# Kernel tuning notes

Measured on AMD Instinct MI355X. Metric: run time of the kernel, lower is better.

Reference implementation:

```python
import jax, jax.numpy as jnp
import numpy as np

N, E, IN_DIM, H_DIM, T = 100000, 3200000, 128, 128, 5000


def gcn_conv(x, W, b, src, dst):
    """PyG GCNConv: symmetric norm with self-loops, linear transform, scatter-add."""
    n = x.shape[0]
    h = x @ W  # [N, h]
    # degree with self-loops (all edge weights = 1)
    deg = jax.ops.segment_sum(jnp.ones(src.shape[0], x.dtype), dst, num_segments=n) + 1.0
    dinv = jax.lax.rsqrt(deg)  # deg >= 1 due to self-loops
    norm = dinv[src] * dinv[dst]  # [E]
    out = jax.ops.segment_sum(h[src] * norm[:, None], dst, num_segments=n)
    out = out + h * (dinv * dinv)[:, None]  # self-loop contribution
    return out + b


def setup_inputs() -> dict:
    key = jax.random.key(0)
    ks = jax.random.split(key, 24)
    s_in = 1.0 / np.sqrt(IN_DIM)
    s_h = 1.0 / np.sqrt(H_DIM)
    return {
        "x": jax.random.normal(ks[0], (N, IN_DIM), jnp.float32),
        "edge_index": jax.random.randint(ks[1], (2, E), 0, N),
        "fake_x": jax.random.normal(ks[2], (N, IN_DIM), jnp.float32),
        "fake_edge_index": jax.random.randint(ks[3], (2, E), 0, N),
        "treat_idx": jax.random.randint(ks[4], (T,), 0, N),
        "control_idx": jax.random.randint(ks[5], (T,), 0, N),
        # GCN layer params
        "W1": jax.random.normal(ks[6], (IN_DIM, H_DIM), jnp.float32) * s_in,
        "b1": jnp.zeros((H_DIM,), jnp.float32),
        "W2": jax.random.normal(ks[7], (H_DIM, H_DIM), jnp.float32) * s_h,
        "b2": jnp.zeros((H_DIM,), jnp.float32),
        # heads
        "Wy1": jax.random.normal(ks[8], (H_DIM, 1), jnp.float32) * s_h,
        "by1": jnp.zeros((1,), jnp.float32),
        "Wy0": jax.random.normal(ks[9], (H_DIM, 1), jnp.float32) * s_h,
        "by0": jnp.zeros((1,), jnp.float32),
        "Wb": jax.random.normal(ks[10], (H_DIM, 2), jnp.float32) * s_h,
        "bb": jnp.zeros((2,), jnp.float32),
        "Wp1": jax.random.normal(ks[11], (H_DIM, H_DIM), jnp.float32) * s_h,
        "bp1": jnp.zeros((H_DIM,), jnp.float32),
        "Wp2": jax.random.normal(ks[12], (H_DIM, 2), jnp.float32) * s_h,
        "bp2": jnp.zeros((2,), jnp.float32),
    }


@jax.custom_vjp
def grl(x):
    return x

def _grl_fwd(x):
    return x, None

def _grl_bwd(_, g):
    return (-g,)

grl.defvjp(_grl_fwd, _grl_bwd)


def reference(x, edge_index, fake_x, fake_edge_index, treat_idx, control_idx,
              W1, b1, W2, b2, Wy1, by1, Wy0, by0, Wb, bb, Wp1, bp1, Wp2, bp2):
    lrelu = jax.nn.leaky_relu  # slope 0.01 matches torch default
    src, dst = edge_index[0], edge_index[1]
    fsrc, fdst = fake_edge_index[0], fake_edge_index[1]

    # layer 1 + relu (dropout is identity in eval mode)
    xZ1 = jax.nn.relu(gcn_conv(x, W1, b1, src, dst))
    xfZ1 = jax.nn.relu(gcn_conv(fake_x, W1, b1, fsrc, fdst))
    # layer 2
    xZ2 = gcn_conv(xZ1, W2, b2, src, dst)
    xfZ2 = gcn_conv(xfZ1, W2, b2, fsrc, fdst)

    y1 = lrelu(xZ2[treat_idx] @ Wy1 + by1).squeeze(-1)
    yc0 = lrelu(xfZ2[treat_idx] @ Wy0 + by0).squeeze(-1)
    y0 = lrelu(xZ2[control_idx] @ Wy0 + by0).squeeze(-1)
    yc1 = lrelu(xfZ2[control_idx] @ Wy1 + by1).squeeze(-1)

    fprob = grl(xZ2) @ Wb + bb
    fprob_f = grl(xfZ2) @ Wb + bb

    tprob = lrelu(lrelu(xZ2 @ Wp1 + bp1) @ Wp2 + bp2)
    tprob_f = lrelu(lrelu(xfZ2 @ Wp1 + bp1) @ Wp2 + bp2)

    return (y1, yc0, y0, yc1, fprob, fprob_f, tprob, tprob_f)
```

## Files before the change

kernel.cpp:

```cpp
#include <hip/hip_runtime.h>

#define DIM 128
#define EPB 8192
#define BINSH 8
#define BINN 256

typedef unsigned int uint32;
typedef __attribute__((ext_vector_type(8))) short short8;
typedef __attribute__((ext_vector_type(4))) float f32x4;

__device__ __forceinline__ uint32 bf16_rtne(float f) {
  uint32 u = __float_as_uint(f);
  return (u + 0x7FFFu + ((u >> 16) & 1u)) >> 16;
}
__device__ __forceinline__ float bf16_to_f(uint32 h) { return __uint_as_float(h << 16); }
__device__ __forceinline__ void unpack2(uint32 u, float& x, float& y) {
  x = __uint_as_float(u << 16);
  y = __uint_as_float(u & 0xFFFF0000u);
}


__launch_bounds__(256)
__global__ void csr_sort_kernel(const int* __restrict__ src, const int* __restrict__ dst,
                                int E, int nb1, uint32* __restrict__ tmp,
                                int* __restrict__ dir) {
  __shared__ uint32 sorted[EPB];
  __shared__ int lcnt[512];
  __shared__ int lbase[512];
  __shared__ int ps[256];
  int t = threadIdx.x;
  int base = blockIdx.x * EPB;

  lcnt[t] = 0;
  lcnt[t + 256] = 0;
  __syncthreads();

  uint32 val[32];
  uint32 br[32];
#pragma unroll
  for (int i = 0; i < 32; ++i) {
    int e = base + i * 256 + t;
    if (e < E) {
      int d = __builtin_nontemporal_load(dst + e);
      int s = __builtin_nontemporal_load(src + e);
      int bin = d >> BINSH;
      val[i] = ((uint32)s << BINSH) | (uint32)(d & (BINN - 1));
      int rank = atomicAdd(&lcnt[bin], 1);
      br[i] = ((uint32)bin << 13) | (uint32)rank;
    } else {
      br[i] = 0xFFFFFFFFu;
    }
  }
  __syncthreads();

  {
    int a0 = lcnt[2 * t], a1 = lcnt[2 * t + 1];
    int psum = a0 + a1;
    ps[t] = psum;
    __syncthreads();
    for (int off = 1; off < 256; off <<= 1) {
      int x = (t >= off) ? ps[t - off] : 0;
      __syncthreads();
      ps[t] += x;
      __syncthreads();
    }
    int ebase = ps[t] - psum;
    lbase[2 * t] = ebase;
    lbase[2 * t + 1] = ebase + a0;
  }
  __syncthreads();

#pragma unroll
  for (int i = 0; i < 32; ++i) {
    if (br[i] != 0xFFFFFFFFu) {
      int bin = br[i] >> 13;
      int rank = br[i] & 0x1FFF;
      sorted[lbase[bin] + rank] = val[i];
    }
  }
  __syncthreads();

  int cnt = min(EPB, E - base);
#pragma unroll
  for (int i = 0; i < 32; ++i) {
    int idx = i * 256 + t;
    if (idx < cnt) tmp[base + idx] = sorted[idx];
  }
  for (int b = t; b <= nb1; b += 256) {
    dir[blockIdx.x * (nb1 + 1) + b] = lbase[b];
  }
}


__launch_bounds__(256)
__global__ void csr_build_kernel(const uint32* __restrict__ tmp, const int* __restrict__ dir,
                                 int nA, int nb1, int N, int binCap,
                                 int* __restrict__ row_beg, int* __restrict__ row_end,
                                 int* __restrict__ cols, float* __restrict__ dinv) {
  __shared__ int rbeg[512];
  __shared__ int rend[512];
  __shared__ int deg[BINN];
  __shared__ int cur[BINN];
  __shared__ int ps[256];
  int j = blockIdx.x;
  int t = threadIdx.x;
  int node0 = j << BINSH;
  int colsBase = j * binCap;

  if (t < BINN) deg[t] = 0;
  for (int i = t; i < nA; i += 256) {
    rbeg[i] = dir[i * (nb1 + 1) + j];
    rend[i] = dir[i * (nb1 + 1) + j + 1];
  }
  __syncthreads();

  for (int i = t; i < nA; i += 256) {
    int b = rbeg[i], en = rend[i];
    for (int q = b; q < en; ++q) {
      atomicAdd(&deg[tmp[(size_t)i * EPB + q] & (BINN - 1)], 1);
    }
  }
  __syncthreads();

  int dv = deg[t];
  ps[t] = dv;
  __syncthreads();
  for (int off = 1; off < 256; off <<= 1) {
    int x = (t >= off) ? ps[t - off] : 0;
    __syncthreads();
    ps[t] += x;
    __syncthreads();
  }
  int ebase = ps[t] - dv;
  cur[t] = ebase;
  int node = node0 + t;
  if (node < N) {
    row_beg[node] = colsBase + ebase;
    row_end[node] = colsBase + ebase + dv;
    dinv[node] = rsqrtf((float)dv + 1.0f);
  }
  __syncthreads();

  for (int i = t; i < nA; i += 256) {
    int b = rbeg[i], en = rend[i];
    for (int q = b; q < en; ++q) {
      uint32 v = tmp[(size_t)i * EPB + q];
      int p = atomicAdd(&cur[v & (BINN - 1)], 1);
      cols[colsBase + p] = (int)(v >> BINSH);
    }
  }
}


__global__ void wsplit_kernel(const float* __restrict__ W, uint4* __restrict__ hi4,
                              uint4* __restrict__ lo4) {
  int tid = blockIdx.x * blockDim.x + threadIdx.x;
  int lane = tid & 63;
  int ks = (tid >> 6) & 3;
  int ct = tid >> 8;
  int col = ct * 16 + (lane & 15);
  int k0 = ks * 32 + ((lane >> 4) << 3);
  uint32 h[8], l[8];
#pragma unroll
  for (int j = 0; j < 8; ++j) {
    float w = W[(size_t)(k0 + j) * DIM + col];
    uint32 hh = bf16_rtne(w);
    float rem = w - bf16_to_f(hh);
    l[j] = bf16_rtne(rem);
    h[j] = hh;
  }
  uint4 H, L;
  H.x = h[0] | (h[1] << 16); H.y = h[2] | (h[3] << 16);
  H.z = h[4] | (h[5] << 16); H.w = h[6] | (h[7] << 16);
  L.x = l[0] | (l[1] << 16); L.y = l[2] | (l[3] << 16);
  L.z = l[4] | (l[5] << 16); L.w = l[6] | (l[7] << 16);
  hi4[tid] = H;
  lo4[tid] = L;
}


__launch_bounds__(256, 3)
__global__ void gemm_mfma_kernel(const float* __restrict__ in, const uint4* __restrict__ wHi,
                                 const uint4* __restrict__ wLo, uint32* __restrict__ outb,
                                 int n, const float* __restrict__ rowscale,
                                 const float* __restrict__ bias, float slope,
                                 const float* __restrict__ headW,
                                 const float* __restrict__ headB,
                                 float* __restrict__ headOut) {
  __shared__ unsigned short sA[2 * 64 * 128];
  __shared__ unsigned short sO[64 * 128];
  int t = threadIdx.x;
  int row0 = blockIdx.x * 64;

  {
    int quad = t & 31;
    int r = t >> 5;
#pragma unroll
    for (int i = 0; i < 8; ++i) {
      int row = r + i * 8;
      int grow = row0 + row;
      f32x4 v = (f32x4){0.f, 0.f, 0.f, 0.f};
      if (grow < n) v = *(const f32x4*)(in + (size_t)grow * DIM + quad * 4);
      uint32 h0 = bf16_rtne(v.x), h1 = bf16_rtne(v.y), h2 = bf16_rtne(v.z), h3 = bf16_rtne(v.w);
      uint32 l0 = bf16_rtne(v.x - bf16_to_f(h0));
      uint32 l1 = bf16_rtne(v.y - bf16_to_f(h1));
      uint32 l2 = bf16_rtne(v.z - bf16_to_f(h2));
      uint32 l3 = bf16_rtne(v.w - bf16_to_f(h3));
      int sidx = (row * 128 + quad * 4) ^ ((row & 7) << 3);
      *(uint2*)&sA[sidx] = make_uint2(h0 | (h1 << 16), h2 | (h3 << 16));
      *(uint2*)&sA[64 * 128 + sidx] = make_uint2(l0 | (l1 << 16), l2 | (l3 << 16));
    }
  }
  __syncthreads();

  int lane = t & 63;
  int w = t >> 6;
  int rbase = w * 16;
  f32x4 acc[8];
#pragma unroll
  for (int ct = 0; ct < 8; ++ct) acc[ct] = (f32x4){0.f, 0.f, 0.f, 0.f};

  int fragRow = rbase + (lane & 15);
  int fragSwz = (fragRow & 7) << 3;
#pragma unroll
  for (int ks = 0; ks < 4; ++ks) {
    int cidx = ks * 32 + ((lane >> 4) << 3);
    int sidx = (fragRow * 128 + cidx) ^ fragSwz;
    uint4 au = *(uint4*)&sA[sidx];
    uint4 alu = *(uint4*)&sA[64 * 128 + sidx];
    short8 ah = __builtin_bit_cast(short8, au);
    short8 al = __builtin_bit_cast(short8, alu);
#pragma unroll
    for (int ct = 0; ct < 8; ++ct) {
      int widx = (ct * 4 + ks) * 64 + lane;
      short8 bh = __builtin_bit_cast(short8, wHi[widx]);
      short8 bl = __builtin_bit_cast(short8, wLo[widx]);
      acc[ct] = __builtin_amdgcn_mfma_f32_16x16x32_bf16(al, bh, acc[ct], 0, 0, 0);
      acc[ct] = __builtin_amdgcn_mfma_f32_16x16x32_bf16(ah, bl, acc[ct], 0, 0, 0);
      acc[ct] = __builtin_amdgcn_mfma_f32_16x16x32_bf16(ah, bh, acc[ct], 0, 0, 0);
    }
  }

  float rs[4];
#pragma unroll
  for (int r = 0; r < 4; ++r) {
    int grow = row0 + rbase + ((lane >> 4) << 2) + r;
    rs[r] = rowscale ? ((grow < n) ? rowscale[grow] : 0.f) : 1.0f;
  }

  float hp0[4] = {0.f, 0.f, 0.f, 0.f};
  float hp1[4] = {0.f, 0.f, 0.f, 0.f};

#pragma unroll
  for (int ct = 0; ct < 8; ++ct) {
    int col = ct * 16 + (lane & 15);
    float bv = bias ? bias[col] : 0.f;
    float hw0 = 0.f, hw1 = 0.f;
    if (headOut) {
      hw0 = headW[col * 2 + 0];
      hw1 = headW[col * 2 + 1];
    }
#pragma unroll
    for (int r = 0; r < 4; ++r) {
      int rowL = rbase + ((lane >> 4) << 2) + r;
      float v = acc[ct][r] * rs[r] + bv;
      v = (v > 0.f) ? v : v * slope;
      if (outb) {
        int sidx = (rowL * 128 + col) ^ ((rowL & 7) << 3);
        sO[sidx] = (unsigned short)bf16_rtne(v);
      }
      if (headOut) {
        hp0[r] = fmaf(v, hw0, hp0[r]);
        hp1[r] = fmaf(v, hw1, hp1[r]);
      }
    }
  }

  if (headOut) {
    float hb0 = headB[0], hb1 = headB[1];
#pragma unroll
    for (int r = 0; r < 4; ++r) {
      float a = hp0[r], b = hp1[r];
#pragma unroll
      for (int off = 8; off; off >>= 1) {
        a += __shfl_xor(a, off);
        b += __shfl_xor(b, off);
      }
      if ((lane & 15) == 0) {
        int grow = row0 + rbase + ((lane >> 4) << 2) + r;
        if (grow < n) {
          float o0 = a + hb0, o1 = b + hb1;
          headOut[2 * (size_t)grow + 0] = (o0 > 0.f) ? o0 : 0.01f * o0;
          headOut[2 * (size_t)grow + 1] = (o1 > 0.f) ? o1 : 0.01f * o1;
        }
      }
    }
  }

  if (outb) {
    __syncthreads();
#pragma unroll
    for (int it = 0; it < 4; ++it) {
      int s = it * 64 + lane;
      int row = rbase + (s >> 4);
      int sin = s & 15;
      int sidx = row * 128 + ((sin * 8) ^ ((row & 7) << 3));
      uint4 v = *(uint4*)&sO[sidx];
      int grow = row0 + row;
      if (grow < n) *(uint4*)(outb + (size_t)grow * 64 + sin * 4) = v;
    }
  }
}


__launch_bounds__(256)
__global__ void agg_kernel(const uint32* __restrict__ g, const int* __restrict__ row_beg,
                           const int* __restrict__ row_end, const int* __restrict__ cols,
                           const float* __restrict__ dinv, const float* __restrict__ bias,
                           float* __restrict__ out, int n, int relu,
                           const float* __restrict__ fpW, const float* __restrict__ fpB,
                           float* __restrict__ fpOut) {
  int lane = threadIdx.x & 63;
  int node = (blockIdx.x * blockDim.x + threadIdx.x) >> 6;
  if (node >= n) return;
  int beg = row_beg[node];
  int end = row_end[node];
  float ax, ay;
  unpack2(g[(size_t)node * 64 + lane], ax, ay);
  float bx = 0.f, by = 0.f;
  int e = beg;
  for (; e + 8 <= end; e += 8) {
    int s0 = cols[e + 0], s1 = cols[e + 1], s2 = cols[e + 2], s3 = cols[e + 3];
    int s4 = cols[e + 4], s5 = cols[e + 5], s6 = cols[e + 6], s7 = cols[e + 7];
    uint32 u0 = g[(size_t)s0 * 64 + lane];
    uint32 u1 = g[(size_t)s1 * 64 + lane];
    uint32 u2 = g[(size_t)s2 * 64 + lane];
    uint32 u3 = g[(size_t)s3 * 64 + lane];
    uint32 u4 = g[(size_t)s4 * 64 + lane];
    uint32 u5 = g[(size_t)s5 * 64 + lane];
    uint32 u6 = g[(size_t)s6 * 64 + lane];
    uint32 u7 = g[(size_t)s7 * 64 + lane];
    float x0, y0, x1, y1, x2, y2, x3, y3, x4, y4, x5, y5, x6, y6, x7, y7;
    unpack2(u0, x0, y0); unpack2(u1, x1, y1);
    unpack2(u2, x2, y2); unpack2(u3, x3, y3);
    unpack2(u4, x4, y4); unpack2(u5, x5, y5);
    unpack2(u6, x6, y6); unpack2(u7, x7, y7);
    ax += (x0 + x1) + (x2 + x3);
    ay += (y0 + y1) + (y2 + y3);
    bx += (x4 + x5) + (x6 + x7);
    by += (y4 + y5) + (y6 + y7);
  }
  for (; e < end; ++e) {
    uint32 u0 = g[(size_t)cols[e] * 64 + lane];
    float x0, y0;
    unpack2(u0, x0, y0);
    ax += x0;
    ay += y0;
  }
  ax += bx;
  ay += by;
  float di = dinv[node];
  float2 bv = ((const float2*)bias)[lane];
  float ox = fmaf(di, ax, bv.x);
  float oy = fmaf(di, ay, bv.y);
  if (relu) {
    ox = fmaxf(ox, 0.f);
    oy = fmaxf(oy, 0.f);
  }
  ((float2*)out)[(size_t)node * 64 + lane] = make_float2(ox, oy);

  if (fpOut) {
    float w00 = fpW[(2 * lane) * 2 + 0];
    float w01 = fpW[(2 * lane) * 2 + 1];
    float w10 = fpW[(2 * lane + 1) * 2 + 0];
    float w11 = fpW[(2 * lane + 1) * 2 + 1];
    float p0 = ox * w00 + oy * w10;
    float p1 = ox * w01 + oy * w11;
#pragma unroll
    for (int off = 32; off; off >>= 1) {
      p0 += __shfl_xor(p0, off);
      p1 += __shfl_xor(p1, off);
    }
    if (lane == 0) {
      fpOut[2 * (size_t)node + 0] = p0 + fpB[0];
      fpOut[2 * (size_t)node + 1] = p1 + fpB[1];
    }
  }
}


__global__ void ydot_kernel(const float* __restrict__ Z, const int* __restrict__ idx,
                            const float* __restrict__ w, const float* __restrict__ b,
                            float* __restrict__ out, int T) {
  int lane = threadIdx.x & 63;
  int t = (blockIdx.x * blockDim.x + threadIdx.x) >> 6;
  if (t >= T) return;
  float2 wv = ((const float2*)w)[lane];
  int node = idx[t];
  float2 z = ((const float2*)Z)[(size_t)node * 64 + lane];
  float pp = z.x * wv.x + z.y * wv.y;
#pragma unroll
  for (int off = 32; off; off >>= 1) pp += __shfl_xor(pp, off);
  if (lane == 0) {
    float o = pp + b[0];
    out[t] = (o > 0.f) ? o : 0.01f * o;
  }
}


extern "C" void kernel_launch(void* const* d_in, const int* in_sizes, int n_in,
                              void* d_out, int out_size, void* d_ws, size_t ws_size,
                              hipStream_t stream) {
  const int N = in_sizes[0] / DIM;
  const int E = in_sizes[1] / 2;
  const int T = in_sizes[4];
  const int nb1 = (N + BINN - 1) >> BINSH;
  const int nA = (E + EPB - 1) / EPB;
  const int binCap = ((E / nb1 + 1024 + 15) / 16) * 16;

  const float* x = (const float*)d_in[0];
  const int* ei = (const int*)d_in[1];
  const float* fx = (const float*)d_in[2];
  const int* fei = (const int*)d_in[3];
  const int* treat = (const int*)d_in[4];
  const int* control = (const int*)d_in[5];
  const float* W1 = (const float*)d_in[6];
  const float* b1 = (const float*)d_in[7];
  const float* W2 = (const float*)d_in[8];
  const float* b2 = (const float*)d_in[9];
  const float* Wy1 = (const float*)d_in[10];
  const float* by1 = (const float*)d_in[11];
  const float* Wy0 = (const float*)d_in[12];
  const float* by0 = (const float*)d_in[13];
  const float* Wb = (const float*)d_in[14];
  const float* bb = (const float*)d_in[15];
  const float* Wp1 = (const float*)d_in[16];
  const float* bp1 = (const float*)d_in[17];
  const float* Wp2 = (const float*)d_in[18];
  const float* bp2 = (const float*)d_in[19];

  float* out = (float*)d_out;

  char* p = (char*)d_ws;
  float* bufZ = (float*)p;   p += (size_t)N * DIM * sizeof(float);
  uint32* bufG = (uint32*)p; p += (size_t)N * (DIM / 2) * sizeof(uint32);
  int* cols = (int*)p;       p += (size_t)nb1 * binCap * sizeof(int);
  int* dir = (int*)p;        p += (size_t)nA * (nb1 + 1) * sizeof(int);
  int* row_beg = (int*)p;    p += (size_t)(N + 16) * sizeof(int);
  int* row_end = (int*)p;    p += (size_t)(N + 16) * sizeof(int);
  float* dinv = (float*)p;   p += (size_t)(N + 16) * sizeof(float);
  uint4* w1Hi = (uint4*)p;   p += 2048 * sizeof(uint4);
  uint4* w1Lo = (uint4*)p;   p += 2048 * sizeof(uint4);
  uint4* w2Hi = (uint4*)p;   p += 2048 * sizeof(uint4);
  uint4* w2Lo = (uint4*)p;   p += 2048 * sizeof(uint4);
  uint4* wp1Hi = (uint4*)p;  p += 2048 * sizeof(uint4);
  uint4* wp1Lo = (uint4*)p;  p += 2048 * sizeof(uint4);
  uint32* tmp = (uint32*)bufZ;

  float* oy1 = out;
  float* oyc0 = out + T;
  float* oy0 = out + 2 * T;
  float* oyc1 = out + 3 * T;
  float* ofp = out + 4 * T;
  float* ofpf = out + 4 * T + 2 * N;
  float* otp = out + 4 * T + 4 * N;
  float* otpf = out + 4 * T + 6 * N;

  wsplit_kernel<<<8, 256, 0, stream>>>(W1, w1Hi, w1Lo);
  wsplit_kernel<<<8, 256, 0, stream>>>(W2, w2Hi, w2Lo);
  wsplit_kernel<<<8, 256, 0, stream>>>(Wp1, wp1Hi, wp1Lo);

  auto run = [&](const float* X, const int* EI,
                 float* y_t, const float* Wt, const float* bt,
                 float* y_c, const float* Wc, const float* bc,
                 float* fp, float* tp) {
    const int* srcp = EI;
    const int* dstp = EI + E;
    csr_sort_kernel<<<nA, 256, 0, stream>>>(srcp, dstp, E, nb1, tmp, dir);
    csr_build_kernel<<<nb1, 256, 0, stream>>>(tmp, dir, nA, nb1, N, binCap,
                                              row_beg, row_end, cols, dinv);
    gemm_mfma_kernel<<<(N + 63) / 64, 256, 0, stream>>>(X, w1Hi, w1Lo, bufG, N, dinv,
                                                        nullptr, 1.0f, nullptr, nullptr, nullptr);
    agg_kernel<<<(N + 3) / 4, 256, 0, stream>>>(bufG, row_beg, row_end, cols, dinv, b1,
                                                bufZ, N, 1, nullptr, nullptr, nullptr);
    gemm_mfma_kernel<<<(N + 63) / 64, 256, 0, stream>>>(bufZ, w2Hi, w2Lo, bufG, N, dinv,
                                                        nullptr, 1.0f, nullptr, nullptr, nullptr);
    agg_kernel<<<(N + 3) / 4, 256, 0, stream>>>(bufG, row_beg, row_end, cols, dinv, b2,
                                                bufZ, N, 0, Wb, bb, fp);
    gemm_mfma_kernel<<<(N + 63) / 64, 256, 0, stream>>>(bufZ, wp1Hi, wp1Lo, nullptr, N, nullptr,
                                                        bp1, 0.01f, Wp2, bp2, tp);
    ydot_kernel<<<(T + 3) / 4, 256, 0, stream>>>(bufZ, treat, Wt, bt, y_t, T);
    ydot_kernel<<<(T + 3) / 4, 256, 0, stream>>>(bufZ, control, Wc, bc, y_c, T);
  };

  run(x, ei, oy1, Wy1, by1, oy0, Wy0, by0, ofp, otp);
  run(fx, fei, oyc0, Wy0, by0, oyc1, Wy1, by1, ofpf, otpf);
}
```

Before: 888.5 us.

## Store layer-1 activations as bf16 and skip lo-split MFMA in layer-2 GEMM

```diff
diff --git a/kernel.cpp b/kernel.cpp
--- a/kernel.cpp
+++ b/kernel.cpp
@@ -183,7 +183,7 @@
 __global__ void gemm_mfma_kernel(const float* __restrict__ in, const uint4* __restrict__ wHi,
                                  const uint4* __restrict__ wLo, uint32* __restrict__ outb,
                                  int n, const float* __restrict__ rowscale,
-                                 const float* __restrict__ bias, float slope,
+                                 const float* __restrict__ bias, float slope, int in_bf16,
                                  const float* __restrict__ headW,
                                  const float* __restrict__ headB,
                                  float* __restrict__ headOut) {
@@ -192,7 +192,20 @@
   int t = threadIdx.x;
   int row0 = blockIdx.x * 64;
 
-  {
+  if (in_bf16) {
+    const uint4* in4 = (const uint4*)in;
+    int q = t & 15;
+    int rl = t >> 4;
+#pragma unroll
+    for (int i = 0; i < 4; ++i) {
+      int row = rl + i * 16;
+      int grow = row0 + row;
+      uint4 v = make_uint4(0, 0, 0, 0);
+      if (grow < n) v = in4[(size_t)grow * 16 + q];
+      int sidx = (row * 128 + q * 8) ^ ((row & 7) << 3);
+      *(uint4*)&sA[sidx] = v;
+    }
+  } else {
     int quad = t & 31;
     int r = t >> 5;
 #pragma unroll
@@ -227,15 +240,15 @@
     int cidx = ks * 32 + ((lane >> 4) << 3);
     int sidx = (fragRow * 128 + cidx) ^ fragSwz;
     uint4 au = *(uint4*)&sA[sidx];
-    uint4 alu = *(uint4*)&sA[64 * 128 + sidx];
     short8 ah = __builtin_bit_cast(short8, au);
-    short8 al = __builtin_bit_cast(short8, alu);
+    short8 al;
+    if (!in_bf16) al = __builtin_bit_cast(short8, *(uint4*)&sA[64 * 128 + sidx]);
 #pragma unroll
     for (int ct = 0; ct < 8; ++ct) {
       int widx = (ct * 4 + ks) * 64 + lane;
       short8 bh = __builtin_bit_cast(short8, wHi[widx]);
       short8 bl = __builtin_bit_cast(short8, wLo[widx]);
-      acc[ct] = __builtin_amdgcn_mfma_f32_16x16x32_bf16(al, bh, acc[ct], 0, 0, 0);
+      if (!in_bf16) acc[ct] = __builtin_amdgcn_mfma_f32_16x16x32_bf16(al, bh, acc[ct], 0, 0, 0);
       acc[ct] = __builtin_amdgcn_mfma_f32_16x16x32_bf16(ah, bl, acc[ct], 0, 0, 0);
       acc[ct] = __builtin_amdgcn_mfma_f32_16x16x32_bf16(ah, bh, acc[ct], 0, 0, 0);
     }
@@ -317,7 +330,7 @@
 __global__ void agg_kernel(const uint32* __restrict__ g, const int* __restrict__ row_beg,
                            const int* __restrict__ row_end, const int* __restrict__ cols,
                            const float* __restrict__ dinv, const float* __restrict__ bias,
-                           float* __restrict__ out, int n, int relu,
+                           void* __restrict__ out, int n, int relu, int out_bf16,
                            const float* __restrict__ fpW, const float* __restrict__ fpB,
                            float* __restrict__ fpOut) {
   int lane = threadIdx.x & 63;
@@ -329,26 +342,38 @@
   unpack2(g[(size_t)node * 64 + lane], ax, ay);
   float bx = 0.f, by = 0.f;
   int e = beg;
-  for (; e + 8 <= end; e += 8) {
-    int s0 = cols[e + 0], s1 = cols[e + 1], s2 = cols[e + 2], s3 = cols[e + 3];
-    int s4 = cols[e + 4], s5 = cols[e + 5], s6 = cols[e + 6], s7 = cols[e + 7];
-    uint32 u0 = g[(size_t)s0 * 64 + lane];
-    uint32 u1 = g[(size_t)s1 * 64 + lane];
-    uint32 u2 = g[(size_t)s2 * 64 + lane];
-    uint32 u3 = g[(size_t)s3 * 64 + lane];
-    uint32 u4 = g[(size_t)s4 * 64 + lane];
-    uint32 u5 = g[(size_t)s5 * 64 + lane];
-    uint32 u6 = g[(size_t)s6 * 64 + lane];
-    uint32 u7 = g[(size_t)s7 * 64 + lane];
-    float x0, y0, x1, y1, x2, y2, x3, y3, x4, y4, x5, y5, x6, y6, x7, y7;
-    unpack2(u0, x0, y0); unpack2(u1, x1, y1);
-    unpack2(u2, x2, y2); unpack2(u3, x3, y3);
-    unpack2(u4, x4, y4); unpack2(u5, x5, y5);
-    unpack2(u6, x6, y6); unpack2(u7, x7, y7);
-    ax += (x0 + x1) + (x2 + x3);
-    ay += (y0 + y1) + (y2 + y3);
-    bx += (x4 + x5) + (x6 + x7);
-    by += (y4 + y5) + (y6 + y7);
+  for (; e + 16 <= end; e += 16) {
+    int s[16];
+#pragma unroll
+    for (int i = 0; i < 16; ++i) s[i] = cols[e + i];
+    uint32 u[16];
+#pragma unroll
+    for (int i = 0; i < 16; ++i) u[i] = g[(size_t)s[i] * 64 + lane];
+#pragma unroll
+    for (int i = 0; i < 16; i += 2) {
+      float x0, y0, x1, y1;
+      unpack2(u[i], x0, y0);
+      unpack2(u[i + 1], x1, y1);
+      ax += x0; ay += y0;
+      bx += x1; by += y1;
+    }
+  }
+  if (e + 8 <= end) {
+    int s[8];
+#pragma unroll
+    for (int i = 0; i < 8; ++i) s[i] = cols[e + i];
+    uint32 u[8];
+#pragma unroll
+    for (int i = 0; i < 8; ++i) u[i] = g[(size_t)s[i] * 64 + lane];
+#pragma unroll
+    for (int i = 0; i < 8; i += 2) {
+      float x0, y0, x1, y1;
+      unpack2(u[i], x0, y0);
+      unpack2(u[i + 1], x1, y1);
+      ax += x0; ay += y0;
+      bx += x1; by += y1;
+    }
+    e += 8;
   }
   for (; e < end; ++e) {
     uint32 u0 = g[(size_t)cols[e] * 64 + lane];
@@ -367,7 +392,12 @@
     ox = fmaxf(ox, 0.f);
     oy = fmaxf(oy, 0.f);
   }
-  ((float2*)out)[(size_t)node * 64 + lane] = make_float2(ox, oy);
+  if (out_bf16) {
+    uint32 pk = bf16_rtne(ox) | (bf16_rtne(oy) << 16);
+    ((uint32*)out)[(size_t)node * 64 + lane] = pk;
+  } else {
+    ((float2*)out)[(size_t)node * 64 + lane] = make_float2(ox, oy);
+  }
 
   if (fpOut) {
     float w00 = fpW[(2 * lane) * 2 + 0];
@@ -480,15 +510,15 @@
     csr_build_kernel<<<nb1, 256, 0, stream>>>(tmp, dir, nA, nb1, N, binCap,
                                               row_beg, row_end, cols, dinv);
     gemm_mfma_kernel<<<(N + 63) / 64, 256, 0, stream>>>(X, w1Hi, w1Lo, bufG, N, dinv,
-                                                        nullptr, 1.0f, nullptr, nullptr, nullptr);
+                                                        nullptr, 1.0f, 0, nullptr, nullptr, nullptr);
     agg_kernel<<<(N + 3) / 4, 256, 0, stream>>>(bufG, row_beg, row_end, cols, dinv, b1,
-                                                bufZ, N, 1, nullptr, nullptr, nullptr);
+                                                (void*)bufZ, N, 1, 1, nullptr, nullptr, nullptr);
     gemm_mfma_kernel<<<(N + 63) / 64, 256, 0, stream>>>(bufZ, w2Hi, w2Lo, bufG, N, dinv,
-                                                        nullptr, 1.0f, nullptr, nullptr, nullptr);
+                                                        nullptr, 1.0f, 1, nullptr, nullptr, nullptr);
     agg_kernel<<<(N + 3) / 4, 256, 0, stream>>>(bufG, row_beg, row_end, cols, dinv, b2,
-                                                bufZ, N, 0, Wb, bb, fp);
+                                                (void*)bufZ, N, 0, 0, Wb, bb, fp);
     gemm_mfma_kernel<<<(N + 63) / 64, 256, 0, stream>>>(bufZ, wp1Hi, wp1Lo, nullptr, N, nullptr,
-                                                        bp1, 0.01f, Wp2, bp2, tp);
+                                                        bp1, 0.01f, 0, Wp2, bp2, tp);
     ydot_kernel<<<(T + 3) / 4, 256, 0, stream>>>(bufZ, treat, Wt, bt, y_t, T);
     ydot_kernel<<<(T + 3) / 4, 256, 0, stream>>>(bufZ, control, Wc, bc, y_c, T);
   };
```

Measured after the change: 875.4 us. About the same (-1.5%).
